# Optimization experiments

Hardware: AMD Instinct MI355X
Metric: run time of the kernel (lower is better)

## Reference

```python
import jax, jax.numpy as jnp
import numpy as np

EPS = 1e-5
TEMP = 0.1

def conv3x3(x, w, b):
    y = jax.lax.conv_general_dilated(x, w, window_strides=(1, 1), padding=((1, 1), (1, 1)),
                                     dimension_numbers=('NCHW', 'OIHW', 'NCHW'))
    return y + b[None, :, None, None]

def batchnorm_train(x, gamma, beta):
    # torch BatchNorm2d training-mode normalization (biased variance)
    mean = jnp.mean(x, axis=(0, 2, 3), keepdims=True)
    var = jnp.var(x, axis=(0, 2, 3), keepdims=True)
    xn = (x - mean) * jax.lax.rsqrt(var + EPS)
    return xn * gamma[None, :, None, None] + beta[None, :, None, None]

def basis_pool(x, pw, pb):
    # x: [B,C,H,W]; pw,pb: [K] (1x1 conv from 1 channel to K basis channels)
    # kernel=stride=2 => non-overlapping 2x2 patches
    B, C, H, W = x.shape
    K = pw.shape[0]
    oh, ow = H // 2, W // 2
    # patches [B,C,oh,ow,4] in (dh,dw) row-major order (matches F.unfold)
    patches = x.reshape(B, C, oh, 2, ow, 2).transpose(0, 1, 2, 4, 3, 5).reshape(B, C, oh, ow, 4)
    # per-channel 1x1 projection -> scores [B,C,K,H,W]
    scores = x[:, :, None] * pw[None, None, :, None, None] + pb[None, None, :, None, None]
    sp = scores.reshape(B, C, K, oh, 2, ow, 2).transpose(0, 1, 2, 3, 5, 4, 6).reshape(B, C, K, oh, ow, 4)
    wts = jax.nn.softmax(sp / TEMP, axis=-1)
    # softmax-weighted sum over the 4 patch elements -> [B,C,K,oh,ow]
    bv = jnp.einsum('bchwp,bckhwp->bckhw', patches, wts)
    # interleave channels as c*K + k (matches torch output layout)
    return bv.reshape(B, C * K, oh, ow)

def setup_inputs() -> dict:
    key = jax.random.key(0)
    ks = jax.random.split(key, 16)
    d = {}
    d['x'] = jax.random.normal(ks[0], (1024, 3, 32, 32), dtype=jnp.float32)
    d['conv1_w'] = jax.random.normal(ks[1], (16, 3, 3, 3), dtype=jnp.float32) * 0.1
    d['conv1_b'] = jax.random.normal(ks[2], (16,), dtype=jnp.float32) * 0.01
    d['bn1_g'] = jnp.ones((16,), jnp.float32)
    d['bn1_b'] = jnp.zeros((16,), jnp.float32)
    d['proj1_w'] = jax.random.normal(ks[3], (2,), dtype=jnp.float32)
    d['proj1_b'] = jax.random.normal(ks[4], (2,), dtype=jnp.float32) * 0.01
    d['conv2_w'] = jax.random.normal(ks[5], (32, 32, 3, 3), dtype=jnp.float32) * 0.06
    d['conv2_b'] = jax.random.normal(ks[6], (32,), dtype=jnp.float32) * 0.01
    d['bn2_g'] = jnp.ones((32,), jnp.float32)
    d['bn2_b'] = jnp.zeros((32,), jnp.float32)
    d['proj2_w'] = jax.random.normal(ks[7], (2,), dtype=jnp.float32)
    d['proj2_b'] = jax.random.normal(ks[8], (2,), dtype=jnp.float32) * 0.01
    d['fc_w'] = jax.random.normal(ks[9], (10, 32 * 2 * 8 * 8), dtype=jnp.float32) * 0.02
    d['fc_b'] = jnp.zeros((10,), jnp.float32)
    return d

def reference(x, conv1_w, conv1_b, bn1_g, bn1_b, proj1_w, proj1_b,
              conv2_w, conv2_b, bn2_g, bn2_b, proj2_w, proj2_b, fc_w, fc_b):
    h = jax.nn.relu(batchnorm_train(conv3x3(x, conv1_w, conv1_b), bn1_g, bn1_b))
    h = basis_pool(h, proj1_w, proj1_b)  # [B,32,16,16]
    h = jax.nn.relu(batchnorm_train(conv3x3(h, conv2_w, conv2_b), bn2_g, bn2_b))
    h = basis_pool(h, proj2_w, proj2_b)  # [B,64,8,8]
    h = h.reshape(h.shape[0], -1)
    return h @ fc_w.T + fc_b
```

## Files before the change

### kernel.cpp

```cpp
#include <hip/hip_runtime.h>

#define EPSV 1e-5f

typedef __attribute__((ext_vector_type(8))) short bf16x8;
typedef __attribute__((ext_vector_type(4))) float f32x4;

__device__ __forceinline__ unsigned short f2bf(float x) {
  unsigned u = __float_as_uint(x);
  unsigned r = (u + 0x7FFFu + ((u >> 16) & 1u)) >> 16;
  return (unsigned short)r;
}

__device__ __forceinline__ float block_reduce_sum(float v, float* lds) {
  #pragma unroll
  for (int off = 32; off > 0; off >>= 1) v += __shfl_down(v, off, 64);
  int lane = threadIdx.x & 63;
  int wid  = threadIdx.x >> 6;
  __syncthreads();
  if (lane == 0) lds[wid] = v;
  __syncthreads();
  float r = 0.f;
  if (threadIdx.x == 0) {
    int nw = blockDim.x >> 6;
    for (int i = 0; i < nw; ++i) r += lds[i];
  }
  return r;
}

__device__ __forceinline__ void stage_x(const float* __restrict__ x, float* xt, int b, int tid) {
  {
    float4* t4 = (float4*)xt;
    #pragma unroll
    for (int i = 0; i < 4; ++i) {
      int idx = i * 256 + tid;
      if (idx < 867) t4[idx] = make_float4(0.f, 0.f, 0.f, 0.f);
    }
  }
  __syncthreads();
  {
    const float4* x4 = (const float4*)(x + b * 3072);
    #pragma unroll
    for (int k = 0; k < 3; ++k) {
      int e4 = k * 256 + tid;
      float4 v = x4[e4];
      int w0 = e4 * 4;
      int ch = w0 >> 10;
      int pos = w0 & 1023;
      int r = pos >> 5, c = pos & 31;
      int base = ch * 1156 + (r + 1) * 34 + (c + 1);
      xt[base] = v.x; xt[base + 1] = v.y; xt[base + 2] = v.z; xt[base + 3] = v.w;
    }
  }
  __syncthreads();
}

__global__ __launch_bounds__(256) void k1_conv1_stats(
    const float* __restrict__ x, const float* __restrict__ w1, const float* __restrict__ b1,
    float* __restrict__ partials ,
    const float* __restrict__ w2, short* __restrict__ wA) {
  __shared__ float xt[3468];
  __shared__ float red[64];
  const int tid = threadIdx.x, b = blockIdx.x;
  const int co0 = blockIdx.y * 8;

  if (b == 0) {
    for (int i = tid + blockIdx.y * 9216; i < (blockIdx.y + 1) * 9216; i += 256) {
      int e = i & 7, l = (i >> 3) & 63, p = (i >> 9) & 1, m = (i >> 10) & 1, s = i >> 11;
      int co = m * 16 + (l & 15);
      int ci = (l >> 4) * 8 + e;
      int ky = s / 3, kx = s - ky * 3;
      float wv = w2[((co * 32 + ci) * 3 + ky) * 3 + kx];
      unsigned short h = f2bf(wv);
      unsigned short val = p ? f2bf(wv - __uint_as_float((unsigned)h << 16)) : h;
      wA[i] = (short)val;
    }
  }

  stage_x(x, xt, b, tid);

  const int c = tid & 31, r0 = (tid >> 5) * 4;
  const int sbase = r0 * 34 + c;
  float xv[54];
  #pragma unroll
  for (int ci = 0; ci < 3; ++ci)
    #pragma unroll
    for (int dr = 0; dr < 6; ++dr)
      #pragma unroll
      for (int dx = 0; dx < 3; ++dx)
        xv[ci * 18 + dr * 3 + dx] = xt[ci * 1156 + sbase + dr * 34 + dx];

  const int lane = tid & 63, wid = tid >> 6;
  #pragma unroll
  for (int cl = 0; cl < 8; ++cl) {
    const int co = co0 + cl;
    float a0, a1, a2, a3;
    a0 = a1 = a2 = a3 = b1[co];
    #pragma unroll
    for (int ci = 0; ci < 3; ++ci)
      #pragma unroll
      for (int ky = 0; ky < 3; ++ky)
        #pragma unroll
        for (int kx = 0; kx < 3; ++kx) {
          float w = w1[co * 27 + ci * 9 + ky * 3 + kx];
          a0 = fmaf(xv[ci * 18 + (0 + ky) * 3 + kx], w, a0);
          a1 = fmaf(xv[ci * 18 + (1 + ky) * 3 + kx], w, a1);
          a2 = fmaf(xv[ci * 18 + (2 + ky) * 3 + kx], w, a2);
          a3 = fmaf(xv[ci * 18 + (3 + ky) * 3 + kx], w, a3);
        }
    float s = a0 + a1 + a2 + a3;
    float q = fmaf(a0, a0, fmaf(a1, a1, fmaf(a2, a2, a3 * a3)));
    #pragma unroll
    for (int o = 32; o > 0; o >>= 1) {
      s += __shfl_down(s, o, 64);
      q += __shfl_down(q, o, 64);
    }
    if (lane == 0) { red[wid * 16 + cl * 2] = s; red[wid * 16 + cl * 2 + 1] = q; }
  }
  __syncthreads();
  if (tid < 16) {
    int cl = tid >> 1, sel = tid & 1;
    float r = red[cl * 2 + sel] + red[16 + cl * 2 + sel] +
              red[32 + cl * 2 + sel] + red[48 + cl * 2 + sel];
    partials[((co0 + cl) * 2 + sel) * 1024 + b] = r;
  }
}

__global__ __launch_bounds__(256) void k_bn_finalize(
    const float* __restrict__ partials, int nb, float invN,
    const float* __restrict__ gamma, const float* __restrict__ beta,
    float* __restrict__ stats, int C) {
  __shared__ float lds[4];
  int c = blockIdx.x;
  float s = 0.f, q = 0.f;
  for (int i = threadIdx.x; i < nb; i += blockDim.x) {
    s += partials[(c * 2 + 0) * nb + i];
    q += partials[(c * 2 + 1) * nb + i];
  }
  s = block_reduce_sum(s, lds);
  q = block_reduce_sum(q, lds);
  if (threadIdx.x == 0) {
    float mean = s * invN;
    float var  = q * invN - mean * mean;
    float scale = gamma[c] * rsqrtf(var + EPSV);
    stats[c]     = scale;
    stats[C + c] = beta[c] - mean * scale;
  }
}

__global__ __launch_bounds__(512, 4) void k34_pool1_conv2(
    const float* __restrict__ x, const float* __restrict__ w1, const float* __restrict__ b1,
    const float* __restrict__ stats1, const float* __restrict__ pw, const float* __restrict__ pb,
    const short* __restrict__ wA, const float* __restrict__ b2,
    float* __restrict__ y2, float* __restrict__ partials) {
  __shared__ __align__(16) short bh[25920];
  const int tid = threadIdx.x, b = blockIdx.x;

  float* xt = (float*)bh;
  {
    float4* t4 = (float4*)xt;
    for (int idx = tid; idx < 867; idx += 512) t4[idx] = make_float4(0.f, 0.f, 0.f, 0.f);
  }
  __syncthreads();
  {
    const float4* x4 = (const float4*)(x + b * 3072);
    for (int e4 = tid; e4 < 768; e4 += 512) {
      float4 v = x4[e4];
      int w0 = e4 * 4;
      int ch = w0 >> 10;
      int pos = w0 & 1023;
      int r = pos >> 5, c = pos & 31;
      int base = ch * 1156 + (r + 1) * 34 + (c + 1);
      xt[base] = v.x; xt[base + 1] = v.y; xt[base + 2] = v.z; xt[base + 3] = v.w;
    }
  }
  __syncthreads();

  const int cell = tid & 255;
  const int chalf = tid >> 8;
  const int ow = cell & 15, oh = cell >> 4;
  const int wbase = (2 * oh) * 34 + 2 * ow;
  float xv[48];
  #pragma unroll
  for (int ci = 0; ci < 3; ++ci)
    #pragma unroll
    for (int dr = 0; dr < 4; ++dr)
      #pragma unroll
      for (int dx = 0; dx < 4; ++dx)
        xv[ci * 16 + dr * 4 + dx] = xt[ci * 1156 + wbase + dr * 34 + dx];
  __syncthreads();

  for (int t = tid; t < 680; t += 512) {
    int plane = t >= 340;
    int u = plane ? t - 340 : t;
    int i = u / 5, part = u - i * 5;
    int r, cc;
    if (i < 18)      { r = 0;  cc = i; }
    else if (i < 36) { r = 17; cc = i - 18; }
    else { int j = i - 36; r = 1 + (j >> 1); cc = (j & 1) * 17; }
    *(int4*)&bh[plane * 12960 + (r * 18 + cc) * 40 + part * 8] = make_int4(0, 0, 0, 0);
  }

  {
    const float pw0 = pw[0] * 10.f, pw1 = pw[1] * 10.f;
    const float pb0 = pb[0] * 10.f, pb1 = pb[1] * 10.f;
    unsigned hiw[8], low[8];
    #pragma unroll
    for (int cl = 0; cl < 8; ++cl) {
      const int c = chalf * 8 + cl;
      const float scale = stats1[c], shift = stats1[16 + c];
      float v[4];
      #pragma unroll
      for (int p = 0; p < 4; ++p) {
        int dh = p >> 1, dw = p & 1;
        float a = b1[c];
        #pragma unroll
        for (int ci = 0; ci < 3; ++ci)
          #pragma unroll
          for (int ky = 0; ky < 3; ++ky)
            #pragma unroll
            for (int kx = 0; kx < 3; ++kx)
              a = fmaf(xv[ci * 16 + (dh + ky) * 4 + (dw + kx)], w1[(c * 3 + ci) * 9 + ky * 3 + kx], a);
        a = fmaf(a, scale, shift);
        v[p] = fmaxf(a, 0.f);
      }
      float o0, o1;
      #pragma unroll
      for (int k = 0; k < 2; ++k) {
        float cw = k ? pw1 : pw0;
        float cb = k ? pb1 : pb0;
        float s0 = fmaf(v[0], cw, cb), s1 = fmaf(v[1], cw, cb);
        float s2 = fmaf(v[2], cw, cb), s3 = fmaf(v[3], cw, cb);
        float m = fmaxf(fmaxf(s0, s1), fmaxf(s2, s3));
        float e0 = expf(s0 - m), e1 = expf(s1 - m), e2 = expf(s2 - m), e3 = expf(s3 - m);
        float den = e0 + e1 + e2 + e3;
        float outv = (v[0] * e0 + v[1] * e1 + v[2] * e2 + v[3] * e3) / den;
        if (k == 0) o0 = outv; else o1 = outv;
      }
      unsigned short h0 = f2bf(o0), h1 = f2bf(o1);
      float f0 = __uint_as_float((unsigned)h0 << 16);
      float f1 = __uint_as_float((unsigned)h1 << 16);
      unsigned short l0 = f2bf(o0 - f0), l1 = f2bf(o1 - f1);
      hiw[cl] = (unsigned)h0 | ((unsigned)h1 << 16);
      low[cl] = (unsigned)l0 | ((unsigned)l1 << 16);
    }
    const int pcell = (oh + 1) * 18 + (ow + 1);
    short* hp = &bh[pcell * 40 + chalf * 16];
    *(int4*)hp       = *(int4*)&hiw[0];
    *(int4*)(hp + 8) = *(int4*)&hiw[4];
    short* lp = &bh[12960 + pcell * 40 + chalf * 16];
    *(int4*)lp       = *(int4*)&low[0];
    *(int4*)(lp + 8) = *(int4*)&low[4];
  }
  __syncthreads();

  const int l = tid & 63;
  const int w = tid >> 6;
  const int q = l >> 4;
  const int c = l & 15;
  const int rbase = w * 2;

  f32x4 acc[2][2];
  #pragma unroll
  for (int m = 0; m < 2; ++m) {
    f32x4 bj = *(const f32x4*)&b2[m * 16 + q * 4];
    acc[m][0] = bj; acc[m][1] = bj;
  }

  const bf16x8* wAf = (const bf16x8*)wA;
  for (int ky = 0; ky < 3; ++ky) {
    for (int kx = 0; kx < 3; ++kx) {
      const int s = ky * 3 + kx;
      bf16x8 a0h = wAf[((s * 2 + 0) * 2 + 0) * 64 + l];
      bf16x8 a0l = wAf[((s * 2 + 0) * 2 + 1) * 64 + l];
      bf16x8 a1h = wAf[((s * 2 + 1) * 2 + 0) * 64 + l];
      bf16x8 a1l = wAf[((s * 2 + 1) * 2 + 1) * 64 + l];
      #pragma unroll
      for (int r = 0; r < 2; ++r) {
        const int pos = (rbase + r + ky) * 18 + (c + kx);
        bf16x8 bhv = *(const bf16x8*)&bh[pos * 40 + q * 8];
        bf16x8 blv = *(const bf16x8*)&bh[12960 + pos * 40 + q * 8];
        acc[0][r] = __builtin_amdgcn_mfma_f32_16x16x32_bf16(a0h, bhv, acc[0][r], 0, 0, 0);
        acc[0][r] = __builtin_amdgcn_mfma_f32_16x16x32_bf16(a0h, blv, acc[0][r], 0, 0, 0);
        acc[0][r] = __builtin_amdgcn_mfma_f32_16x16x32_bf16(a0l, bhv, acc[0][r], 0, 0, 0);
        acc[1][r] = __builtin_amdgcn_mfma_f32_16x16x32_bf16(a1h, bhv, acc[1][r], 0, 0, 0);
        acc[1][r] = __builtin_amdgcn_mfma_f32_16x16x32_bf16(a1h, blv, acc[1][r], 0, 0, 0);
        acc[1][r] = __builtin_amdgcn_mfma_f32_16x16x32_bf16(a1l, bhv, acc[1][r], 0, 0, 0);
      }
    }
  }

  {
    float* yb = y2 + b * 8192;
    #pragma unroll
    for (int m = 0; m < 2; ++m)
      #pragma unroll
      for (int r = 0; r < 2; ++r)
        #pragma unroll
        for (int j = 0; j < 4; ++j)
          yb[(m * 16 + q * 4 + j) * 256 + (rbase + r) * 16 + c] = acc[m][r][j];
  }

  const int slot = b * 8 + w;
  #pragma unroll
  for (int m = 0; m < 2; ++m) {
    #pragma unroll
    for (int j = 0; j < 4; ++j) {
      float a0 = acc[m][0][j], a1 = acc[m][1][j];
      float sv = a0 + a1;
      float qv = fmaf(a0, a0, a1 * a1);
      #pragma unroll
      for (int o = 1; o <= 8; o <<= 1) {
        sv += __shfl_xor(sv, o, 64);
        qv += __shfl_xor(qv, o, 64);
      }
      if (c == 0) {
        int co = m * 16 + q * 4 + j;
        partials[(co * 2 + 0) * 8192 + slot] = sv;
        partials[(co * 2 + 1) * 8192 + slot] = qv;
      }
    }
  }
}

__global__ __launch_bounds__(256) void k78_pool2_fc(
    const float* __restrict__ y2, const float* __restrict__ stats2,
    const float* __restrict__ pw, const float* __restrict__ pb,
    const float* __restrict__ fcw, const float* __restrict__ fcb,
    float* __restrict__ out) {
  __shared__ float h2s[4096];
  __shared__ float red[40];
  const int tid = threadIdx.x;
  const int b = blockIdx.x;

  {
    const int c = tid >> 3, oh = tid & 7;
    const float scale = stats2[c], shift = stats2[32 + c];
    const float pw0 = pw[0] * 10.f, pw1 = pw[1] * 10.f;
    const float pb0 = pb[0] * 10.f, pb1 = pb[1] * 10.f;
    const float* yb = y2 + (b * 32 + c) * 256 + (2 * oh) * 16;
    float rowa[16], rowb[16];
    #pragma unroll
    for (int k = 0; k < 4; ++k) {
      *(float4*)&rowa[k * 4] = ((const float4*)yb)[k];
      *(float4*)&rowb[k * 4] = ((const float4*)(yb + 16))[k];
    }
    #pragma unroll
    for (int ow = 0; ow < 8; ++ow) {
      float v0 = fmaxf(fmaf(rowa[2 * ow],     scale, shift), 0.f);
      float v1 = fmaxf(fmaf(rowa[2 * ow + 1], scale, shift), 0.f);
      float v2 = fmaxf(fmaf(rowb[2 * ow],     scale, shift), 0.f);
      float v3 = fmaxf(fmaf(rowb[2 * ow + 1], scale, shift), 0.f);
      #pragma unroll
      for (int k = 0; k < 2; ++k) {
        float cw = k ? pw1 : pw0;
        float cb = k ? pb1 : pb0;
        float s0 = fmaf(v0, cw, cb), s1 = fmaf(v1, cw, cb);
        float s2 = fmaf(v2, cw, cb), s3 = fmaf(v3, cw, cb);
        float m = fmaxf(fmaxf(s0, s1), fmaxf(s2, s3));
        float e0 = expf(s0 - m), e1 = expf(s1 - m), e2 = expf(s2 - m), e3 = expf(s3 - m);
        float den = e0 + e1 + e2 + e3;
        h2s[(c * 2 + k) * 64 + oh * 8 + ow] =
            (v0 * e0 + v1 * e1 + v2 * e2 + v3 * e3) / den;
      }
    }
  }
  __syncthreads();

  float acc[10];
  #pragma unroll
  for (int j = 0; j < 10; ++j) acc[j] = 0.f;
  #pragma unroll
  for (int k = 0; k < 16; ++k) {
    float hv = h2s[k * 256 + tid];
    #pragma unroll
    for (int j = 0; j < 10; ++j)
      acc[j] = fmaf(hv, fcw[j * 4096 + k * 256 + tid], acc[j]);
  }
  const int lane = tid & 63, wid = tid >> 6;
  #pragma unroll
  for (int j = 0; j < 10; ++j) {
    float v = acc[j];
    #pragma unroll
    for (int off = 32; off > 0; off >>= 1) v += __shfl_down(v, off, 64);
    if (lane == 0) red[wid * 10 + j] = v;
  }
  __syncthreads();
  if (tid < 10) {
    out[b * 10 + tid] = red[tid] + red[10 + tid] + red[20 + tid] + red[30 + tid] + fcb[tid];
  }
}

extern "C" void kernel_launch(void* const* d_in, const int* in_sizes, int n_in,
                              void* d_out, int out_size, void* d_ws, size_t ws_size,
                              hipStream_t stream) {
  (void)in_sizes; (void)n_in; (void)out_size; (void)ws_size;
  const float* x   = (const float*)d_in[0];
  const float* w1  = (const float*)d_in[1];
  const float* b1  = (const float*)d_in[2];
  const float* g1  = (const float*)d_in[3];
  const float* be1 = (const float*)d_in[4];
  const float* pw1 = (const float*)d_in[5];
  const float* pb1 = (const float*)d_in[6];
  const float* w2  = (const float*)d_in[7];
  const float* b2  = (const float*)d_in[8];
  const float* g2  = (const float*)d_in[9];
  const float* be2 = (const float*)d_in[10];
  const float* pw2 = (const float*)d_in[11];
  const float* pb2 = (const float*)d_in[12];
  const float* fcw = (const float*)d_in[13];
  const float* fcb = (const float*)d_in[14];
  float* out = (float*)d_out;

  char* ws = (char*)d_ws;
  float* y2       = (float*)(ws);
  float* partials = (float*)(ws + 33554432);
  short* wA       = (short*)(ws + 33554432 + 2097152);
  float* stats1   = (float*)(ws + 33554432 + 2097152 + 36864);
  float* stats2   = stats1 + 32;

  dim3 g2d(1024, 2);
  k1_conv1_stats<<<g2d, 256, 0, stream>>>(x, w1, b1, partials, w2, wA);
  k_bn_finalize<<<16, 256, 0, stream>>>(partials, 1024, 1.f / 1048576.f, g1, be1, stats1, 16);
  k34_pool1_conv2<<<1024, 512, 0, stream>>>(x, w1, b1, stats1, pw1, pb1, wA, b2, y2, partials);
  k_bn_finalize<<<32, 256, 0, stream>>>(partials, 8192, 1.f / 262144.f, g2, be2, stats2, 32);
  k78_pool2_fc<<<1024, 256, 0, stream>>>(y2, stats2, pw2, pb2, fcw, fcb, out);
}
```

Baseline: 107.6 us.

## Store conv1 output instead of recomputing it in pool1/conv2 kernel

The first kernel now writes the pre-BN conv1 activations to a new 64MB workspace buffer in channel-last layout. The pool1/conv2 kernel reads them back instead of restaging the input and recomputing the 3x3 conv. The softmax exponentials switch to the fast __expf intrinsic, and the second occupancy hint is dropped from the launch bounds. This trades recompute FLOPs for a large extra round trip through global memory.

New measurement: 119.1 us. 10.8% more time.

```diff
diff --git a/kernel.cpp b/kernel.cpp
--- a/kernel.cpp
+++ b/kernel.cpp
@@ -57,7 +57,7 @@
 __global__ __launch_bounds__(256) void k1_conv1_stats(
     const float* __restrict__ x, const float* __restrict__ w1, const float* __restrict__ b1,
     float* __restrict__ partials ,
-    const float* __restrict__ w2, short* __restrict__ wA) {
+    const float* __restrict__ w2, short* __restrict__ wA, float* __restrict__ y1) {
   __shared__ float xt[3468];
   __shared__ float red[64];
   const int tid = threadIdx.x, b = blockIdx.x;
@@ -90,6 +90,7 @@
         xv[ci * 18 + dr * 3 + dx] = xt[ci * 1156 + sbase + dr * 34 + dx];
 
   const int lane = tid & 63, wid = tid >> 6;
+  float st0[8], st1[8], st2[8], st3[8];
   #pragma unroll
   for (int cl = 0; cl < 8; ++cl) {
     const int co = co0 + cl;
@@ -107,6 +108,7 @@
           a2 = fmaf(xv[ci * 18 + (2 + ky) * 3 + kx], w, a2);
           a3 = fmaf(xv[ci * 18 + (3 + ky) * 3 + kx], w, a3);
         }
+    st0[cl] = a0; st1[cl] = a1; st2[cl] = a2; st3[cl] = a3;
     float s = a0 + a1 + a2 + a3;
     float q = fmaf(a0, a0, fmaf(a1, a1, fmaf(a2, a2, a3 * a3)));
     #pragma unroll
@@ -116,6 +118,19 @@
     }
     if (lane == 0) { red[wid * 16 + cl * 2] = s; red[wid * 16 + cl * 2 + 1] = q; }
   }
+
+  {
+    float* yb = y1 + (size_t)b * 16384 + co0;
+    *(float4*)(yb + ((r0 + 0) * 32 + c) * 16)     = *(float4*)&st0[0];
+    *(float4*)(yb + ((r0 + 0) * 32 + c) * 16 + 4) = *(float4*)&st0[4];
+    *(float4*)(yb + ((r0 + 1) * 32 + c) * 16)     = *(float4*)&st1[0];
+    *(float4*)(yb + ((r0 + 1) * 32 + c) * 16 + 4) = *(float4*)&st1[4];
+    *(float4*)(yb + ((r0 + 2) * 32 + c) * 16)     = *(float4*)&st2[0];
+    *(float4*)(yb + ((r0 + 2) * 32 + c) * 16 + 4) = *(float4*)&st2[4];
+    *(float4*)(yb + ((r0 + 3) * 32 + c) * 16)     = *(float4*)&st3[0];
+    *(float4*)(yb + ((r0 + 3) * 32 + c) * 16 + 4) = *(float4*)&st3[4];
+  }
+
   __syncthreads();
   if (tid < 16) {
     int cl = tid >> 1, sel = tid & 1;
@@ -147,47 +162,13 @@
   }
 }
 
-__global__ __launch_bounds__(512, 4) void k34_pool1_conv2(
-    const float* __restrict__ x, const float* __restrict__ w1, const float* __restrict__ b1,
-    const float* __restrict__ stats1, const float* __restrict__ pw, const float* __restrict__ pb,
+__global__ __launch_bounds__(512) void k34_pool1_conv2(
+    const float* __restrict__ y1, const float* __restrict__ stats1,
+    const float* __restrict__ pw, const float* __restrict__ pb,
     const short* __restrict__ wA, const float* __restrict__ b2,
     float* __restrict__ y2, float* __restrict__ partials) {
   __shared__ __align__(16) short bh[25920];
   const int tid = threadIdx.x, b = blockIdx.x;
-
-  float* xt = (float*)bh;
-  {
-    float4* t4 = (float4*)xt;
-    for (int idx = tid; idx < 867; idx += 512) t4[idx] = make_float4(0.f, 0.f, 0.f, 0.f);
-  }
-  __syncthreads();
-  {
-    const float4* x4 = (const float4*)(x + b * 3072);
-    for (int e4 = tid; e4 < 768; e4 += 512) {
-      float4 v = x4[e4];
-      int w0 = e4 * 4;
-      int ch = w0 >> 10;
-      int pos = w0 & 1023;
-      int r = pos >> 5, c = pos & 31;
-      int base = ch * 1156 + (r + 1) * 34 + (c + 1);
-      xt[base] = v.x; xt[base + 1] = v.y; xt[base + 2] = v.z; xt[base + 3] = v.w;
-    }
-  }
-  __syncthreads();
-
-  const int cell = tid & 255;
-  const int chalf = tid >> 8;
-  const int ow = cell & 15, oh = cell >> 4;
-  const int wbase = (2 * oh) * 34 + 2 * ow;
-  float xv[48];
-  #pragma unroll
-  for (int ci = 0; ci < 3; ++ci)
-    #pragma unroll
-    for (int dr = 0; dr < 4; ++dr)
-      #pragma unroll
-      for (int dx = 0; dx < 4; ++dx)
-        xv[ci * 16 + dr * 4 + dx] = xt[ci * 1156 + wbase + dr * 34 + dx];
-  __syncthreads();
 
   for (int t = tid; t < 680; t += 512) {
     int plane = t >= 340;
@@ -200,6 +181,20 @@
     *(int4*)&bh[plane * 12960 + (r * 18 + cc) * 40 + part * 8] = make_int4(0, 0, 0, 0);
   }
 
+  const int cell = tid & 255;
+  const int chalf = tid >> 8;
+  const int ow = cell & 15, oh = cell >> 4;
+  const float* yb = y1 + (size_t)b * 16384 + ((2 * oh) * 32 + 2 * ow) * 16 + chalf * 8;
+  float va[8], vb[8], vc[8], vd[8];
+  *(float4*)&va[0] = *(const float4*)(yb);
+  *(float4*)&va[4] = *(const float4*)(yb + 4);
+  *(float4*)&vb[0] = *(const float4*)(yb + 16);
+  *(float4*)&vb[4] = *(const float4*)(yb + 20);
+  *(float4*)&vc[0] = *(const float4*)(yb + 512);
+  *(float4*)&vc[4] = *(const float4*)(yb + 516);
+  *(float4*)&vd[0] = *(const float4*)(yb + 528);
+  *(float4*)&vd[4] = *(const float4*)(yb + 532);
+
   {
     const float pw0 = pw[0] * 10.f, pw1 = pw[1] * 10.f;
     const float pb0 = pb[0] * 10.f, pb1 = pb[1] * 10.f;
@@ -208,32 +203,22 @@
     for (int cl = 0; cl < 8; ++cl) {
       const int c = chalf * 8 + cl;
       const float scale = stats1[c], shift = stats1[16 + c];
-      float v[4];
-      #pragma unroll
-      for (int p = 0; p < 4; ++p) {
-        int dh = p >> 1, dw = p & 1;
-        float a = b1[c];
-        #pragma unroll
-        for (int ci = 0; ci < 3; ++ci)
-          #pragma unroll
-          for (int ky = 0; ky < 3; ++ky)
-            #pragma unroll
-            for (int kx = 0; kx < 3; ++kx)
-              a = fmaf(xv[ci * 16 + (dh + ky) * 4 + (dw + kx)], w1[(c * 3 + ci) * 9 + ky * 3 + kx], a);
-        a = fmaf(a, scale, shift);
-        v[p] = fmaxf(a, 0.f);
-      }
+      float v0 = fmaxf(fmaf(va[cl], scale, shift), 0.f);
+      float v1 = fmaxf(fmaf(vb[cl], scale, shift), 0.f);
+      float v2 = fmaxf(fmaf(vc[cl], scale, shift), 0.f);
+      float v3 = fmaxf(fmaf(vd[cl], scale, shift), 0.f);
       float o0, o1;
       #pragma unroll
       for (int k = 0; k < 2; ++k) {
         float cw = k ? pw1 : pw0;
         float cb = k ? pb1 : pb0;
-        float s0 = fmaf(v[0], cw, cb), s1 = fmaf(v[1], cw, cb);
-        float s2 = fmaf(v[2], cw, cb), s3 = fmaf(v[3], cw, cb);
+        float s0 = fmaf(v0, cw, cb), s1 = fmaf(v1, cw, cb);
+        float s2 = fmaf(v2, cw, cb), s3 = fmaf(v3, cw, cb);
         float m = fmaxf(fmaxf(s0, s1), fmaxf(s2, s3));
-        float e0 = expf(s0 - m), e1 = expf(s1 - m), e2 = expf(s2 - m), e3 = expf(s3 - m);
+        float e0 = __expf(s0 - m), e1 = __expf(s1 - m);
+        float e2 = __expf(s2 - m), e3 = __expf(s3 - m);
         float den = e0 + e1 + e2 + e3;
-        float outv = (v[0] * e0 + v[1] * e1 + v[2] * e2 + v[3] * e3) / den;
+        float outv = (v0 * e0 + v1 * e1 + v2 * e2 + v3 * e3) / den;
         if (k == 0) o0 = outv; else o1 = outv;
       }
       unsigned short h0 = f2bf(o0), h1 = f2bf(o1);
@@ -290,14 +275,14 @@
   }
 
   {
-    float* yb = y2 + b * 8192;
+    float* yb2 = y2 + b * 8192;
     #pragma unroll
     for (int m = 0; m < 2; ++m)
       #pragma unroll
       for (int r = 0; r < 2; ++r)
         #pragma unroll
         for (int j = 0; j < 4; ++j)
-          yb[(m * 16 + q * 4 + j) * 256 + (rbase + r) * 16 + c] = acc[m][r][j];
+          yb2[(m * 16 + q * 4 + j) * 256 + (rbase + r) * 16 + c] = acc[m][r][j];
   }
 
   const int slot = b * 8 + w;
@@ -357,7 +342,8 @@
         float s0 = fmaf(v0, cw, cb), s1 = fmaf(v1, cw, cb);
         float s2 = fmaf(v2, cw, cb), s3 = fmaf(v3, cw, cb);
         float m = fmaxf(fmaxf(s0, s1), fmaxf(s2, s3));
-        float e0 = expf(s0 - m), e1 = expf(s1 - m), e2 = expf(s2 - m), e3 = expf(s3 - m);
+        float e0 = __expf(s0 - m), e1 = __expf(s1 - m);
+        float e2 = __expf(s2 - m), e3 = __expf(s3 - m);
         float den = e0 + e1 + e2 + e3;
         h2s[(c * 2 + k) * 64 + oh * 8 + ow] =
             (v0 * e0 + v1 * e1 + v2 * e2 + v3 * e3) / den;
@@ -412,16 +398,17 @@
   float* out = (float*)d_out;
 
   char* ws = (char*)d_ws;
-  float* y2       = (float*)(ws);
-  float* partials = (float*)(ws + 33554432);
-  short* wA       = (short*)(ws + 33554432 + 2097152);
-  float* stats1   = (float*)(ws + 33554432 + 2097152 + 36864);
+  float* y1       = (float*)(ws);
+  float* y2       = (float*)(ws + 67108864);
+  float* partials = (float*)(ws + 67108864 + 33554432);
+  short* wA       = (short*)(ws + 67108864 + 33554432 + 2097152);
+  float* stats1   = (float*)(ws + 67108864 + 33554432 + 2097152 + 36864);
   float* stats2   = stats1 + 32;
 
   dim3 g2d(1024, 2);
-  k1_conv1_stats<<<g2d, 256, 0, stream>>>(x, w1, b1, partials, w2, wA);
+  k1_conv1_stats<<<g2d, 256, 0, stream>>>(x, w1, b1, partials, w2, wA, y1);
   k_bn_finalize<<<16, 256, 0, stream>>>(partials, 1024, 1.f / 1048576.f, g1, be1, stats1, 16);
-  k34_pool1_conv2<<<1024, 512, 0, stream>>>(x, w1, b1, stats1, pw1, pb1, wA, b2, y2, partials);
+  k34_pool1_conv2<<<1024, 512, 0, stream>>>(y1, stats1, pw1, pb1, wA, b2, y2, partials);
   k_bn_finalize<<<32, 256, 0, stream>>>(partials, 8192, 1.f / 262144.f, g2, be2, stats2, 32);
   k78_pool2_fc<<<1024, 256, 0, stream>>>(y2, stats2, pw2, pb2, fcw, fcb, out);
 }
```
